# Kernel tuning notes

Measured on AMD Instinct MI355X. Metric: run time of the kernel, lower is better.

## Reference

```python
import math
import jax, jax.numpy as jnp
import numpy as np


def setup_inputs() -> dict:
    key = jax.random.key(0)
    k1, k2 = jax.random.split(key)
    N, H, W, h, d = 32, 32, 32, 16, 64
    input_NHWhd = jax.random.normal(k1, (N, H, W, h, d), dtype=jnp.float32)
    emb_2dd = jax.random.uniform(k2, (2, d, d), dtype=jnp.float32) * (2.0 * math.pi)
    return {"input_NHWhd": input_NHWhd, "emb_2dd": emb_2dd}


def _positions(H, W):
    # xlim = sqrt(W/H), ylim = sqrt(H/W); positions stacked as (y, x)
    xlim = math.sqrt(W / H)
    ylim = math.sqrt(H / W)
    x_HW = jnp.broadcast_to(jnp.linspace(-xlim, xlim, W, dtype=jnp.float32)[None, :], (H, W))
    y_HW = jnp.broadcast_to(jnp.linspace(-ylim, ylim, H, dtype=jnp.float32)[:, None], (H, W))
    return jnp.stack((y_HW, x_HW), axis=-1)  # [H, W, 2]


def reference(input_NHWhd, emb_2dd):
    N, H, W, h, d = input_NHWhd.shape
    # skew-symmetric generator bases (the -0.5 shift cancels in M - M^T,
    # kept for faithfulness to the original)
    upper_2dd = jnp.triu(emb_2dd, k=1) - 0.5
    skew_2dd = upper_2dd - jnp.swapaxes(upper_2dd, -2, -1)  # [2, d, d]
    pos_HW2 = _positions(H, W)
    # per-position generator: sum over the 2 spatial components
    gen_HWdd = jnp.einsum("hwc,cij->hwij", pos_HW2, skew_2dd)  # [H, W, d, d]
    rot_HWdd = jax.vmap(jax.scipy.linalg.expm)(gen_HWdd.reshape(-1, d, d)).reshape(H, W, d, d)
    # apply rotation: out[n,y,x,q,:] = input[n,y,x,q,:] @ rot[y,x]
    out_NHWhd = jnp.einsum("nhwqd,hwde->nhwqe", input_NHWhd, rot_HWdd.astype(input_NHWhd.dtype))
    return out_NHWhd
```

## Files before the change

### kernel.cpp

```cpp
#include <hip/hip_runtime.h>


typedef float f4 __attribute__((ext_vector_type(4)));
typedef short s8v __attribute__((ext_vector_type(8)));
typedef float f32x4 __attribute__((ext_vector_type(4)));

constexpr int LST = 68;
constexpr int BST = 72;

static __device__ __forceinline__ unsigned short f2bf(float f) {
    unsigned int u = __float_as_uint(f);
    u += 0x7fffu + ((u >> 16) & 1u);
    return (unsigned short)(u >> 16);
}

static __device__ __forceinline__ void mm(float* __restrict__ C,
                                          const float* __restrict__ A,
                                          const float* __restrict__ B,
                                          float cI, int tid) {
    const int r0 = (tid >> 4) << 2;
    const int c0 = (tid & 15) << 2;
    f4 acc0 = {0.f, 0.f, 0.f, 0.f}, acc1 = acc0, acc2 = acc0, acc3 = acc0;
#pragma unroll 4
    for (int k = 0; k < 64; k += 4) {
        f4 b0 = *(const f4*)&B[(k + 0) * LST + c0];
        f4 b1 = *(const f4*)&B[(k + 1) * LST + c0];
        f4 b2 = *(const f4*)&B[(k + 2) * LST + c0];
        f4 b3 = *(const f4*)&B[(k + 3) * LST + c0];
        f4 a0 = *(const f4*)&A[(r0 + 0) * LST + k];
        f4 a1 = *(const f4*)&A[(r0 + 1) * LST + k];
        f4 a2 = *(const f4*)&A[(r0 + 2) * LST + k];
        f4 a3 = *(const f4*)&A[(r0 + 3) * LST + k];
        acc0 += a0.x * b0; acc0 += a0.y * b1; acc0 += a0.z * b2; acc0 += a0.w * b3;
        acc1 += a1.x * b0; acc1 += a1.y * b1; acc1 += a1.z * b2; acc1 += a1.w * b3;
        acc2 += a2.x * b0; acc2 += a2.y * b1; acc2 += a2.z * b2; acc2 += a2.w * b3;
        acc3 += a3.x * b0; acc3 += a3.y * b1; acc3 += a3.z * b2; acc3 += a3.w * b3;
    }
    if (r0 == c0) { acc0.x += cI; acc1.y += cI; acc2.z += cI; acc3.w += cI; }
    *(f4*)&C[(r0 + 0) * LST + c0] = acc0;
    *(f4*)&C[(r0 + 1) * LST + c0] = acc1;
    *(f4*)&C[(r0 + 2) * LST + c0] = acc2;
    *(f4*)&C[(r0 + 3) * LST + c0] = acc3;
}

__global__ __launch_bounds__(256, 2)
void liere_fused(const float* __restrict__ in, const float* __restrict__ emb,
                 float* __restrict__ out) {
    __shared__ __align__(16) float sA[64 * LST];
    __shared__ __align__(16) float sU[64 * LST];
    __shared__ __align__(16) float sV[64 * LST];
    __shared__ float snorm;

    const int tid = threadIdx.x;
    const int p = blockIdx.x;
    const int y = p >> 5;
    const int x = p & 31;

#pragma unroll
    for (int i = 0; i < 4; ++i) {
        int lin = i * 1024 + tid * 4;
        int r = lin >> 6, c = lin & 63;
        *(f4*)&sU[r * LST + c] = *(const f4*)&emb[lin];
        *(f4*)&sV[r * LST + c] = *(const f4*)&emb[4096 + lin];
    }
    __syncthreads();

    const float yv = (2.0f * (float)y - 31.0f) / 31.0f;
    const float xv = (2.0f * (float)x - 31.0f) / 31.0f;
    {
        const int r0 = (tid >> 4) << 2, c0 = (tid & 15) << 2;
#pragma unroll
        for (int i = 0; i < 4; ++i)
#pragma unroll
            for (int j = 0; j < 4; ++j) {
                int r = r0 + i, c = c0 + j;
                float s0, s1;
                if (r < c)      { s0 = sU[r * LST + c];  s1 = sV[r * LST + c]; }
                else if (r > c) { s0 = -sU[c * LST + r]; s1 = -sV[c * LST + r]; }
                else            { s0 = 0.f; s1 = 0.f; }
                sA[r * LST + c] = yv * s0 + xv * s1;
            }
    }
    __syncthreads();

    if (tid < 64) {
        float s = 0.f;
        for (int c = 0; c < 64; ++c) s += fabsf(sA[tid * LST + c]);
#pragma unroll
        for (int off = 32; off > 0; off >>= 1) s = fmaxf(s, __shfl_down(s, off, 64));
        if (tid == 0) snorm = s;
    }
    __syncthreads();
    int sq = 0;
    {
        float nm = snorm;
        if (nm > 1.0f) sq = (int)ceilf(log2f(nm));
        if (sq < 0) sq = 0;
        if (sq > 14) sq = 14;
    }
    const float scale = exp2f((float)(-sq));

    const float C9 = 2.75573192e-6f, C8 = 2.48015876e-5f, C7 = 1.98412701e-4f,
                C6 = 1.38888893e-3f, C5 = 8.33333377e-3f, C4 = 4.16666679e-2f,
                C3 = 0.166666672f,   C2 = 0.5f,           C1 = 1.0f, C0 = 1.0f;

    {
        const int r0 = (tid >> 4) << 2, c0 = (tid & 15) << 2;
#pragma unroll
        for (int i = 0; i < 4; ++i)
#pragma unroll
            for (int j = 0; j < 4; ++j) {
                int r = r0 + i, c = c0 + j;
                float a = sA[r * LST + c] * scale;
                sA[r * LST + c] = a;
                sU[r * LST + c] = C9 * a + ((r == c) ? C8 : 0.f);
            }
    }
    __syncthreads();

    mm(sV, sU, sA, C7, tid); __syncthreads();
    mm(sU, sV, sA, C6, tid); __syncthreads();
    mm(sV, sU, sA, C5, tid); __syncthreads();
    mm(sU, sV, sA, C4, tid); __syncthreads();
    mm(sV, sU, sA, C3, tid); __syncthreads();
    mm(sU, sV, sA, C2, tid); __syncthreads();
    mm(sV, sU, sA, C1, tid); __syncthreads();
    mm(sU, sV, sA, C0, tid); __syncthreads();

    float* cur = sU;
    float* oth = sV;
    for (int i = 0; i < sq; ++i) {
        mm(oth, cur, cur, 0.f, tid);
        __syncthreads();
        float* t = cur; cur = oth; oth = t;
    }

    unsigned short* Rb = (unsigned short*)sA;
    unsigned short* RT = (unsigned short*)oth;
    {
        const int r = tid >> 2;
        const int k0 = (tid & 3) << 4;
        for (int k = k0; k < k0 + 16; ++k) {
            unsigned short b = f2bf(cur[r * LST + k]);
            Rb[r * BST + k] = b;
            RT[k * BST + r] = b;
        }
    }
    __syncthreads();

    const int w = tid >> 6;
    const int lane = tid & 63;
    const int m = lane & 15;
    const int q4 = lane >> 4;
    const int pass = w >> 1;
    const int nbase = (w & 1) << 4;

    const unsigned short* RF = pass ? Rb : RT;
    s8v rf[4][2];
#pragma unroll
    for (int t = 0; t < 4; ++t) {
        rf[t][0] = *(const s8v*)&RF[(t * 16 + m) * BST + q4 * 8];
        rf[t][1] = *(const s8v*)&RF[(t * 16 + m) * BST + 32 + q4 * 8];
    }

    const int yy = pass ? (31 - y) : y;
    const int xx = pass ? (31 - x) : x;
    const size_t pos = (size_t)(yy * 32 + xx) * 1024;

    for (int i = 0; i < 16; ++i) {
        const int n = nbase + i;
        const size_t nb = (size_t)n << 20;
        const float* src = in + nb + pos + m * 64 + q4 * 8;
        f4 u0 = *(const f4*)src;
        f4 u1 = *(const f4*)(src + 4);
        f4 u2 = *(const f4*)(src + 32);
        f4 u3 = *(const f4*)(src + 36);
        s8v b0, b1;
        b0[0] = (short)f2bf(u0.x); b0[1] = (short)f2bf(u0.y);
        b0[2] = (short)f2bf(u0.z); b0[3] = (short)f2bf(u0.w);
        b0[4] = (short)f2bf(u1.x); b0[5] = (short)f2bf(u1.y);
        b0[6] = (short)f2bf(u1.z); b0[7] = (short)f2bf(u1.w);
        b1[0] = (short)f2bf(u2.x); b1[1] = (short)f2bf(u2.y);
        b1[2] = (short)f2bf(u2.z); b1[3] = (short)f2bf(u2.w);
        b1[4] = (short)f2bf(u3.x); b1[5] = (short)f2bf(u3.y);
        b1[6] = (short)f2bf(u3.z); b1[7] = (short)f2bf(u3.w);

        f32x4 acc0 = {0.f,0.f,0.f,0.f}, acc1 = acc0, acc2 = acc0, acc3 = acc0;
        acc0 = __builtin_amdgcn_mfma_f32_16x16x32_bf16(rf[0][0], b0, acc0, 0, 0, 0);
        acc0 = __builtin_amdgcn_mfma_f32_16x16x32_bf16(rf[0][1], b1, acc0, 0, 0, 0);
        acc1 = __builtin_amdgcn_mfma_f32_16x16x32_bf16(rf[1][0], b0, acc1, 0, 0, 0);
        acc1 = __builtin_amdgcn_mfma_f32_16x16x32_bf16(rf[1][1], b1, acc1, 0, 0, 0);
        acc2 = __builtin_amdgcn_mfma_f32_16x16x32_bf16(rf[2][0], b0, acc2, 0, 0, 0);
        acc2 = __builtin_amdgcn_mfma_f32_16x16x32_bf16(rf[2][1], b1, acc2, 0, 0, 0);
        acc3 = __builtin_amdgcn_mfma_f32_16x16x32_bf16(rf[3][0], b0, acc3, 0, 0, 0);
        acc3 = __builtin_amdgcn_mfma_f32_16x16x32_bf16(rf[3][1], b1, acc3, 0, 0, 0);

        float* dst = out + nb + pos + m * 64 + q4 * 4;
        f4 o0 = {acc0[0], acc0[1], acc0[2], acc0[3]};
        f4 o1 = {acc1[0], acc1[1], acc1[2], acc1[3]};
        f4 o2 = {acc2[0], acc2[1], acc2[2], acc2[3]};
        f4 o3 = {acc3[0], acc3[1], acc3[2], acc3[3]};
        *(f4*)(dst +  0) = o0;
        *(f4*)(dst + 16) = o1;
        *(f4*)(dst + 32) = o2;
        *(f4*)(dst + 48) = o3;
    }
}

extern "C" void kernel_launch(void* const* d_in, const int* in_sizes, int n_in,
                              void* d_out, int out_size, void* d_ws, size_t ws_size,
                              hipStream_t stream) {
    (void)in_sizes; (void)n_in; (void)out_size; (void)d_ws; (void)ws_size;
    const float* in = (const float*)d_in[0];
    const float* emb = (const float*)d_in[1];
    float* out = (float*)d_out;
    hipLaunchKernelGGL(liere_fused, dim3(512), dim3(256), 0, stream, in, emb, out);
}
```

Baseline: 283.8 us.

## Compute matrix exponential with split-bf16 MFMA instead of scalar FP32 LDS matmuls

Replaces the FP32 FMA-based 64x64 matmuls of the Horner polynomial and the squaring steps with MFMA bf16 instructions. Each operand is split into high and low bf16 parts, and three MFMA products per k-step approximate FP32 accuracy. Matrices are stored transposed in bf16 LDS slots, and an explicit transpose is added after each squaring. This is meant to cut the per-block setup cost of the expm, at the price of extra LDS transposes and some accuracy risk from dropping the low-times-low term.

```diff
diff --git a/kernel.cpp b/kernel.cpp
--- a/kernel.cpp
+++ b/kernel.cpp
@@ -4,57 +4,128 @@
 typedef float f4 __attribute__((ext_vector_type(4)));
 typedef short s8v __attribute__((ext_vector_type(8)));
 typedef float f32x4 __attribute__((ext_vector_type(4)));
+typedef unsigned short ush;
+typedef unsigned int u32;
+typedef ush us4 __attribute__((ext_vector_type(4)));
 
 constexpr int LST = 68;
 constexpr int BST = 72;
-
-static __device__ __forceinline__ unsigned short f2bf(float f) {
-    unsigned int u = __float_as_uint(f);
+constexpr int SLOT = 64 * BST;
+
+static __device__ __forceinline__ ush f2bf(float f) {
+    u32 u = __float_as_uint(f);
     u += 0x7fffu + ((u >> 16) & 1u);
-    return (unsigned short)(u >> 16);
-}
-
-static __device__ __forceinline__ void mm(float* __restrict__ C,
-                                          const float* __restrict__ A,
-                                          const float* __restrict__ B,
-                                          float cI, int tid) {
-    const int r0 = (tid >> 4) << 2;
-    const int c0 = (tid & 15) << 2;
-    f4 acc0 = {0.f, 0.f, 0.f, 0.f}, acc1 = acc0, acc2 = acc0, acc3 = acc0;
-#pragma unroll 4
-    for (int k = 0; k < 64; k += 4) {
-        f4 b0 = *(const f4*)&B[(k + 0) * LST + c0];
-        f4 b1 = *(const f4*)&B[(k + 1) * LST + c0];
-        f4 b2 = *(const f4*)&B[(k + 2) * LST + c0];
-        f4 b3 = *(const f4*)&B[(k + 3) * LST + c0];
-        f4 a0 = *(const f4*)&A[(r0 + 0) * LST + k];
-        f4 a1 = *(const f4*)&A[(r0 + 1) * LST + k];
-        f4 a2 = *(const f4*)&A[(r0 + 2) * LST + k];
-        f4 a3 = *(const f4*)&A[(r0 + 3) * LST + k];
-        acc0 += a0.x * b0; acc0 += a0.y * b1; acc0 += a0.z * b2; acc0 += a0.w * b3;
-        acc1 += a1.x * b0; acc1 += a1.y * b1; acc1 += a1.z * b2; acc1 += a1.w * b3;
-        acc2 += a2.x * b0; acc2 += a2.y * b1; acc2 += a2.z * b2; acc2 += a2.w * b3;
-        acc3 += a3.x * b0; acc3 += a3.y * b1; acc3 += a3.z * b2; acc3 += a3.w * b3;
-    }
-    if (r0 == c0) { acc0.x += cI; acc1.y += cI; acc2.z += cI; acc3.w += cI; }
-    *(f4*)&C[(r0 + 0) * LST + c0] = acc0;
-    *(f4*)&C[(r0 + 1) * LST + c0] = acc1;
-    *(f4*)&C[(r0 + 2) * LST + c0] = acc2;
-    *(f4*)&C[(r0 + 3) * LST + c0] = acc3;
+    return (ush)(u >> 16);
+}
+static __device__ __forceinline__ float bf2f(ush h) {
+    return __uint_as_float(((u32)h) << 16);
+}
+static __device__ __forceinline__ s8v negbf(s8v v) {
+    u32* p = (u32*)&v;
+#pragma unroll
+    for (int i = 0; i < 4; ++i) p[i] ^= 0x80008000u;
+    return v;
+}
+
+static __device__ __forceinline__ void load_frag(
+    s8v fr[2][2][2], const ush* __restrict__ ah, const ush* __restrict__ al,
+    int m, int q4, int base, bool neg)
+{
+#pragma unroll
+    for (int t = 0; t < 2; ++t)
+#pragma unroll
+        for (int ks = 0; ks < 2; ++ks) {
+            const int off = (base + t * 16 + m) * BST + ks * 32 + q4 * 8;
+            s8v h = *(const s8v*)&ah[off];
+            s8v l = *(const s8v*)&al[off];
+            if (neg) { h = negbf(h); l = negbf(l); }
+            fr[t][ks][0] = h;
+            fr[t][ks][1] = l;
+        }
+}
+
+static __device__ __forceinline__ void mm_pre(
+    ush* __restrict__ dh, ush* __restrict__ dl,
+    const s8v pa[2][2][2],
+    const ush* __restrict__ qh, const ush* __restrict__ ql,
+    float cdiag, int m, int q4, int DM, int DN)
+{
+    s8v qb[2][2][2];
+    load_frag(qb, qh, ql, m, q4, DN, false);
+
+    f32x4 acc[2][2];
+#pragma unroll
+    for (int mt = 0; mt < 2; ++mt)
+#pragma unroll
+        for (int nt = 0; nt < 2; ++nt) acc[mt][nt] = (f32x4){0.f, 0.f, 0.f, 0.f};
+
+#pragma unroll
+    for (int ks = 0; ks < 2; ++ks)
+#pragma unroll
+        for (int mt = 0; mt < 2; ++mt)
+#pragma unroll
+            for (int nt = 0; nt < 2; ++nt) {
+                acc[mt][nt] = __builtin_amdgcn_mfma_f32_16x16x32_bf16(
+                    pa[mt][ks][0], qb[nt][ks][0], acc[mt][nt], 0, 0, 0);
+                acc[mt][nt] = __builtin_amdgcn_mfma_f32_16x16x32_bf16(
+                    pa[mt][ks][0], qb[nt][ks][1], acc[mt][nt], 0, 0, 0);
+                acc[mt][nt] = __builtin_amdgcn_mfma_f32_16x16x32_bf16(
+                    pa[mt][ks][1], qb[nt][ks][0], acc[mt][nt], 0, 0, 0);
+            }
+
+#pragma unroll
+    for (int mt = 0; mt < 2; ++mt)
+#pragma unroll
+        for (int nt = 0; nt < 2; ++nt) {
+            const int gm = DM + mt * 16 + q4 * 4;
+            const int gn = DN + nt * 16 + m;
+            us4 h4, l4;
+#pragma unroll
+            for (int r = 0; r < 4; ++r) {
+                float v = acc[mt][nt][r];
+                if (gn == gm + r) v += cdiag;
+                const ush h = f2bf(v);
+                h4[r] = h;
+                l4[r] = f2bf(v - bf2f(h));
+            }
+            *(us4*)&dh[gn * BST + gm] = h4;
+            *(us4*)&dl[gn * BST + gm] = l4;
+        }
+}
+
+static __device__ __forceinline__ void transp(
+    ush* __restrict__ dh, ush* __restrict__ dl,
+    const ush* __restrict__ sh, const ush* __restrict__ sl, int tid)
+{
+    const int r = tid & 63;
+    const int k0 = (tid >> 6) << 4;
+    s8v a0 = *(const s8v*)&sh[r * BST + k0];
+    s8v a1 = *(const s8v*)&sh[r * BST + k0 + 8];
+    s8v b0 = *(const s8v*)&sl[r * BST + k0];
+    s8v b1 = *(const s8v*)&sl[r * BST + k0 + 8];
+#pragma unroll
+    for (int j = 0; j < 8; ++j) {
+        dh[(k0 + j) * BST + r]     = ((const ush*)&a0)[j];
+        dh[(k0 + j + 8) * BST + r] = ((const ush*)&a1)[j];
+        dl[(k0 + j) * BST + r]     = ((const ush*)&b0)[j];
+        dl[(k0 + j + 8) * BST + r] = ((const ush*)&b1)[j];
+    }
 }
 
 __global__ __launch_bounds__(256, 2)
 void liere_fused(const float* __restrict__ in, const float* __restrict__ emb,
                  float* __restrict__ out) {
-    __shared__ __align__(16) float sA[64 * LST];
-    __shared__ __align__(16) float sU[64 * LST];
-    __shared__ __align__(16) float sV[64 * LST];
+    __shared__ __align__(16) ush buf[6 * SLOT];
     __shared__ float snorm;
 
     const int tid = threadIdx.x;
     const int p = blockIdx.x;
     const int y = p >> 5;
     const int x = p & 31;
+
+    float* sG = (float*)(buf);
+    float* sU = (float*)(buf + 2 * SLOT);
+    float* sV = (float*)(buf + 4 * SLOT);
 
 #pragma unroll
     for (int i = 0; i < 4; ++i) {
@@ -78,14 +149,14 @@
                 if (r < c)      { s0 = sU[r * LST + c];  s1 = sV[r * LST + c]; }
                 else if (r > c) { s0 = -sU[c * LST + r]; s1 = -sV[c * LST + r]; }
                 else            { s0 = 0.f; s1 = 0.f; }
-                sA[r * LST + c] = yv * s0 + xv * s1;
+                sG[r * LST + c] = yv * s0 + xv * s1;
             }
     }
     __syncthreads();
 
     if (tid < 64) {
         float s = 0.f;
-        for (int c = 0; c < 64; ++c) s += fabsf(sA[tid * LST + c]);
+        for (int c = 0; c < 64; ++c) s += fabsf(sG[tid * LST + c]);
 #pragma unroll
         for (int off = 32; off > 0; off >>= 1) s = fmaxf(s, __shfl_down(s, off, 64));
         if (tid == 0) snorm = s;
@@ -104,6 +175,10 @@
                 C6 = 1.38888893e-3f, C5 = 8.33333377e-3f, C4 = 4.16666679e-2f,
                 C3 = 0.166666672f,   C2 = 0.5f,           C1 = 1.0f, C0 = 1.0f;
 
+    ush* Xh = buf + 2 * SLOT;  ush* Xl = buf + 3 * SLOT;
+    ush* t_h = buf + 4 * SLOT; ush* t_l = buf + 5 * SLOT;
+    ush* u_h = buf + 0 * SLOT; ush* u_l = buf + 1 * SLOT;
+
     {
         const int r0 = (tid >> 4) << 2, c0 = (tid & 15) << 2;
 #pragma unroll
@@ -111,51 +186,55 @@
 #pragma unroll
             for (int j = 0; j < 4; ++j) {
                 int r = r0 + i, c = c0 + j;
-                float a = sA[r * LST + c] * scale;
-                sA[r * LST + c] = a;
-                sU[r * LST + c] = C9 * a + ((r == c) ? C8 : 0.f);
-            }
-    }
-    __syncthreads();
-
-    mm(sV, sU, sA, C7, tid); __syncthreads();
-    mm(sU, sV, sA, C6, tid); __syncthreads();
-    mm(sV, sU, sA, C5, tid); __syncthreads();
-    mm(sU, sV, sA, C4, tid); __syncthreads();
-    mm(sV, sU, sA, C3, tid); __syncthreads();
-    mm(sU, sV, sA, C2, tid); __syncthreads();
-    mm(sV, sU, sA, C1, tid); __syncthreads();
-    mm(sU, sV, sA, C0, tid); __syncthreads();
-
-    float* cur = sU;
-    float* oth = sV;
-    for (int i = 0; i < sq; ++i) {
-        mm(oth, cur, cur, 0.f, tid);
-        __syncthreads();
-        float* t = cur; cur = oth; oth = t;
-    }
-
-    unsigned short* Rb = (unsigned short*)sA;
-    unsigned short* RT = (unsigned short*)oth;
-    {
-        const int r = tid >> 2;
-        const int k0 = (tid & 3) << 4;
-        for (int k = k0; k < k0 + 16; ++k) {
-            unsigned short b = f2bf(cur[r * LST + k]);
-            Rb[r * BST + k] = b;
-            RT[k * BST + r] = b;
-        }
-    }
-    __syncthreads();
-
+                float a = sG[r * LST + c] * scale;
+                ush xh = f2bf(a);
+                Xh[r * BST + c] = xh;
+                Xl[r * BST + c] = f2bf(a - bf2f(xh));
+                float t0 = C9 * a + ((r == c) ? C8 : 0.f);
+                ush th = f2bf(t0);
+                t_h[r * BST + c] = th;
+                t_l[r * BST + c] = f2bf(t0 - bf2f(th));
+            }
+    }
+    __syncthreads();
+
+    const int lane = tid & 63;
     const int w = tid >> 6;
-    const int lane = tid & 63;
     const int m = lane & 15;
     const int q4 = lane >> 4;
+    const int DM = (w & 1) * 32;
+    const int DN = (w >> 1) * 32;
+
+    s8v xf[2][2][2];
+    load_frag(xf, Xh, Xl, m, q4, DM, true);
+
+    const float cs[8] = {C7, C6, C5, C4, C3, C2, C1, C0};
+#pragma unroll
+    for (int s = 0; s < 8; ++s) {
+        mm_pre(u_h, u_l, xf, t_h, t_l, cs[s], m, q4, DM, DN);
+        __syncthreads();
+        ush* th2 = t_h; t_h = u_h; u_h = th2;
+        ush* tl2 = t_l; t_l = u_l; u_l = tl2;
+    }
+    ush* tt_h = Xh; ush* tt_l = Xl;
+    transp(tt_h, tt_l, t_h, t_l, tid);
+    __syncthreads();
+
+    for (int i = 0; i < sq; ++i) {
+        s8v af[2][2][2];
+        load_frag(af, tt_h, tt_l, m, q4, DM, false);
+        mm_pre(u_h, u_l, af, t_h, t_l, 0.f, m, q4, DM, DN);
+        __syncthreads();
+        transp(tt_h, tt_l, u_h, u_l, tid);
+        __syncthreads();
+        ush* th2 = t_h; t_h = u_h; u_h = th2;
+        ush* tl2 = t_l; t_l = u_l; u_l = tl2;
+    }
+
     const int pass = w >> 1;
     const int nbase = (w & 1) << 4;
 
-    const unsigned short* RF = pass ? Rb : RT;
+    const ush* RF = pass ? t_h : tt_h;
     s8v rf[4][2];
 #pragma unroll
     for (int t = 0; t < 4; ++t) {
```

Result: faster. 263.6 us (-7.1%).
